# Performance work log

Hardware: AMD Instinct MI355X
Metric: run time of the kernel (lower is better)

Reference implementation:

```python
import jax, jax.numpy as jnp
import numpy as np

N_NODES = 100000
N_EDGES = 800000
EDGE_NAMES = ["ei_connected_to", "ei_ordered_next", "ei_represents", "ei_represented_by",
              "ei_neighboring_vertical", "ei_neighboring_horizontal", "ei_contains",
              "ei_order", "ei_perpendicular"]
AGGRS_L2 = ["sum", "sum", "mean", "mean", "sum", "sum", "mean"]


def _glorot(key, shape):
    fan_in, fan_out = shape[-2], shape[-1]
    s = (2.0 / (fan_in + fan_out)) ** 0.5
    return jax.random.normal(key, shape, dtype=jnp.float32) * s


def setup_inputs() -> dict:
    key = jax.random.key(0)
    ks = iter(jax.random.split(key, 32))
    inp = {"x": jax.random.normal(next(ks), (N_NODES, 6), dtype=jnp.float32)}
    for name in EDGE_NAMES:
        inp[name] = jax.random.randint(next(ks), (2, N_EDGES), 0, N_NODES, dtype=jnp.int32)
    inp.update(
        W0n=_glorot(next(ks), (2, 6, 16)), W0r=_glorot(next(ks), (2, 6, 16)),
        b0=jnp.zeros((2, 16), jnp.float32),
        W1n=_glorot(next(ks), (2, 16, 32)), W1r=_glorot(next(ks), (2, 16, 32)),
        b1=jnp.zeros((2, 32), jnp.float32),
        P1=_glorot(next(ks), (16, 32)), pb1=jnp.zeros((32,), jnp.float32),
        W2n=_glorot(next(ks), (7, 32, 64)), W2r=_glorot(next(ks), (7, 32, 64)),
        b2=jnp.zeros((7, 64), jnp.float32),
        P2=_glorot(next(ks), (32, 64)), pb2=jnp.zeros((64,), jnp.float32),
    )
    return inp


def _hetero_conv(x, edges, aggrs, Wn, Wr, b):
    # Per-relation GraphConv: out_d = aggr(x[src]->dst) @ Wn_r + x @ Wr_r + b_r,
    # summed across relations (HeteroConv aggr='sum'). Loop is over a small fixed
    # set of relation types (structurally distinct), not data dims.
    n = x.shape[0]
    out = jnp.zeros((n, Wn.shape[-1]), x.dtype)
    for i, (ei, aggr) in enumerate(zip(edges, aggrs)):
        src, dst = ei[0], ei[1]
        msg = jax.ops.segment_sum(x[src], dst, num_segments=n)  # scatter-add gather
        if aggr == "mean":
            cnt = jax.ops.segment_sum(jnp.ones_like(dst, dtype=x.dtype), dst, num_segments=n)
            msg = msg / jnp.maximum(cnt, 1.0)[:, None]
        out = out + msg @ Wn[i] + x @ Wr[i] + b[i]
    return out


def reference(x, W0n, W0r, b0, W1n, W1r, b1, P1, pb1, W2n, W2r, b2, P2, pb2,
              ei_connected_to, ei_ordered_next, ei_represents, ei_represented_by,
              ei_neighboring_vertical, ei_neighboring_horizontal, ei_contains,
              ei_order, ei_perpendicular):
    e01 = [ei_connected_to, ei_ordered_next]
    e2 = [ei_represents, ei_represented_by, ei_neighboring_vertical,
          ei_neighboring_horizontal, ei_contains, ei_order, ei_perpendicular]
    # local head: 6 -> 16 (two sum relations)
    h = _hetero_conv(x, e01, ["sum", "sum"], W0n, W0r, b0)
    # residual block 1: 16 -> 32 (same two sum relations, linear residual projection)
    h = jax.nn.relu(_hetero_conv(h, e01, ["sum", "sum"], W1n, W1r, b1) + h @ P1 + pb1)
    # residual block 2: 32 -> 64 (seven relations, sum/mean aggregation)
    h = jax.nn.relu(_hetero_conv(h, e2, AGGRS_L2, W2n, W2r, b2) + h @ P2 + pb2)
    # final elementwise relu from SemanticModule.forward
    return jax.nn.relu(h)
```

## Files before the change

### kernel.cpp

```cpp
#include <hip/hip_runtime.h>

#define NN 100000
#define NE 800000
#define NRG 256
#define SPAN 392
#define CAP 4096
#define NBIN (9 * NRG)
#define ACH 2048

typedef _Float16 f16;
typedef __attribute__((ext_vector_type(4))) _Float16 f16x4;
typedef __attribute__((ext_vector_type(8))) _Float16 f16x8;
typedef __attribute__((ext_vector_type(4))) float f32x4;
typedef __attribute__((ext_vector_type(2))) float f32x2;

#define NTL(p) __builtin_nontemporal_load(p)

struct EPtrs { const int* s[9]; const int* d[9]; };

__global__ __launch_bounds__(256) void prep_weights(
    const float* __restrict__ W0n, const float* __restrict__ W0r, const float* __restrict__ b0,
    const float* __restrict__ W1n, const float* __restrict__ W1r, const float* __restrict__ b1,
    const float* __restrict__ P1,  const float* __restrict__ pb1,
    const float* __restrict__ W2n, const float* __restrict__ W2r, const float* __restrict__ b2,
    const float* __restrict__ P2,  const float* __restrict__ pb2,
    float* __restrict__ wc0, float* __restrict__ bc0,
    float* __restrict__ wc1, float* __restrict__ bc1,
    f16*   __restrict__ b2frag, float* __restrict__ bc2,
    int*   __restrict__ cursor)
{
    int gtid = blockIdx.x * 256 + threadIdx.x;
    int gstr = gridDim.x * 256;

    for (int t = gtid; t < NBIN; t += gstr) cursor[t] = 0;

    for (int t = gtid; t < 18 * 16; t += gstr) {
        int row = t >> 4, col = t & 15;
        float v;
        if (row < 6)       v = W0n[row * 16 + col];
        else if (row < 12) v = W0n[96 + (row - 6) * 16 + col];
        else               v = W0r[(row - 12) * 16 + col] + W0r[96 + (row - 12) * 16 + col];
        wc0[t] = v;
    }
    for (int t = gtid; t < 16; t += gstr) bc0[t] = b0[t] + b0[16 + t];

    for (int t = gtid; t < 48 * 32; t += gstr) {
        int row = t >> 5, col = t & 31;
        float v;
        if (row < 16)      v = W1n[row * 32 + col];
        else if (row < 32) v = W1n[512 + (row - 16) * 32 + col];
        else { int rr = row - 32; v = W1r[rr * 32 + col] + W1r[512 + rr * 32 + col] + P1[rr * 32 + col]; }
        wc1[t] = v;
    }
    for (int t = gtid; t < 32; t += gstr) bc1[t] = b1[t] + b1[32 + t] + pb1[t];

    for (int t = gtid; t < 256 * 64; t += gstr) {
        int j = t & 7, lane = (t >> 3) & 63, ntk = t >> 9;
        int nt = ntk & 3, kt = ntk >> 2;
        int k = kt * 32 + (lane >> 4) * 8 + j;
        int n = nt * 16 + (lane & 15);
        float v;
        if (k < 224) v = W2n[k * 64 + n];
        else {
            int rr = k - 224;
            v = P2[rr * 64 + n];
            #pragma unroll
            for (int r = 0; r < 7; ++r) v += W2r[r * 2048 + rr * 64 + n];
        }
        b2frag[t] = (f16)v;
    }
    for (int t = gtid; t < 64; t += gstr) {
        float v = pb2[t];
        #pragma unroll
        for (int r = 0; r < 7; ++r) v += b2[r * 64 + t];
        bc2[t] = v;
    }
}

__global__ __launch_bounds__(256) void passA(EPtrs ep, int* __restrict__ cursor,
                                             unsigned* __restrict__ binbuf)
{
    int r = blockIdx.y;
    int e0 = blockIdx.x * ACH;
    int cnt = min(ACH, NE - e0);
    int tid = threadIdx.x;
    __shared__ int h[NRG];
    __shared__ int bs[NRG];
    __shared__ int gb[NRG];
    __shared__ int wsumA[4];
    __shared__ unsigned pk[ACH];
    __shared__ unsigned char pkb[ACH];

    h[tid] = 0;
    __syncthreads();

    const int* dp = ep.d[r];
    const int* sp = ep.s[r];
    unsigned wv[8];
    int rgk[8];
    int lrk[8];
    #pragma unroll
    for (int k = 0; k < 8; ++k) {
        int e = e0 + k * 256 + tid;
        rgk[k] = -1;
        if (e < NE) {
            int d = NTL(dp + e);
            int sv = NTL(sp + e);
            int g = d / SPAN;
            int l = d - g * SPAN;
            wv[k] = ((unsigned)l << 17) | (unsigned)sv;
            rgk[k] = g;
            lrk[k] = atomicAdd(&h[g], 1);
        }
    }
    __syncthreads();

    int vcnt = h[tid];
    int lane = tid & 63, wid = tid >> 6;
    int incl = vcnt;
    #pragma unroll
    for (int ofs = 1; ofs < 64; ofs <<= 1) {
        int u = __shfl_up(incl, ofs, 64);
        if (lane >= ofs) incl += u;
    }
    if (lane == 63) wsumA[wid] = incl;
    __syncthreads();
    if (tid == 0) {
        int a = wsumA[0], b = wsumA[1], c = wsumA[2];
        wsumA[0] = 0; wsumA[1] = a; wsumA[2] = a + b; wsumA[3] = a + b + c;
    }
    __syncthreads();
    int excl = incl - vcnt + wsumA[wid];
    bs[tid] = excl;
    gb[tid] = (vcnt > 0) ? atomicAdd(&cursor[r * NRG + tid], vcnt) : 0;
    __syncthreads();

    #pragma unroll
    for (int k = 0; k < 8; ++k) {
        if (rgk[k] >= 0) {
            int p = bs[rgk[k]] + lrk[k];
            pk[p] = wv[k];
            pkb[p] = (unsigned char)rgk[k];
        }
    }
    __syncthreads();

    for (int i = tid; i < cnt; i += 256) {
        int g = pkb[i];
        int pos = gb[g] + (i - bs[g]);
        if (pos < CAP)
            binbuf[((size_t)(r * NRG + g)) * CAP + pos] = pk[i];
    }
}

__global__ __launch_bounds__(256) void passB(const unsigned* __restrict__ binbuf,
                                             const int* __restrict__ cursor,
                                             int* __restrict__ deg, int* __restrict__ off,
                                             int* __restrict__ eidx)
{
    int bin = blockIdx.x;
    int r = bin >> 8, rg = bin & (NRG - 1);
    int lo = rg * SPAN;
    int n_here = min(SPAN, NN - lo);
    int tid = threadIdx.x;
    __shared__ int h[SPAN];
    __shared__ int wsum[4];
    __shared__ int stage[CAP];

    int sz = min(cursor[bin], CAP);
    const unsigned* bp = binbuf + (size_t)bin * CAP;

    for (int i = tid; i < SPAN; i += 256) h[i] = 0;
    __syncthreads();

    unsigned wv[16];
    int rk[16];
    #pragma unroll
    for (int k = 0; k < 16; ++k) {
        int e = tid + k * 256;
        if (e < sz) {
            unsigned w = NTL(bp + e);
            wv[k] = w;
            rk[k] = atomicAdd(&h[w >> 17], 1);
        }
    }
    __syncthreads();

    int i0 = tid * 2;
    int dstash[2];
    int s = 0;
    #pragma unroll
    for (int k = 0; k < 2; ++k) {
        int i = i0 + k;
        int v = (i < SPAN) ? h[i] : 0;
        dstash[k] = v;
        s += v;
    }
    int lane = tid & 63, wid = tid >> 6;
    int incl = s;
    #pragma unroll
    for (int ofs = 1; ofs < 64; ofs <<= 1) {
        int u = __shfl_up(incl, ofs, 64);
        if (lane >= ofs) incl += u;
    }
    if (lane == 63) wsum[wid] = incl;
    __syncthreads();
    if (tid == 0) {
        int a = wsum[0], b = wsum[1], c = wsum[2];
        wsum[0] = 0; wsum[1] = a; wsum[2] = a + b; wsum[3] = a + b + c;
    }
    __syncthreads();
    int run = incl - s + wsum[wid];
    int base = bin * CAP;
    #pragma unroll
    for (int k = 0; k < 2; ++k) {
        int i = i0 + k;
        if (i < SPAN) {
            int v = dstash[k];
            h[i] = run;
            if (i < n_here) {
                deg[r * NN + lo + i] = v;
                off[r * NN + lo + i] = base + run + v;
            }
            run += v;
        }
    }
    __syncthreads();

    #pragma unroll
    for (int k = 0; k < 16; ++k) {
        int e = tid + k * 256;
        if (e < sz) {
            unsigned w = wv[k];
            stage[h[w >> 17] + rk[k]] = (int)(w & 0x1FFFF);
        }
    }
    __syncthreads();
    for (int i = tid; i < sz; i += 256) eidx[base + i] = stage[i];
}

__global__ __launch_bounds__(256) void t0f(const float* __restrict__ x,
                                           const int* __restrict__ deg, const int* __restrict__ off,
                                           const int* __restrict__ eidx,
                                           const float* __restrict__ wc0, const float* __restrict__ bc0,
                                           f16* __restrict__ h0h)
{
    __shared__ float sw[288 + 16];
    for (int t = threadIdx.x; t < 304; t += 256) sw[t] = (t < 288) ? wc0[t] : bc0[t - 288];
    __syncthreads();
    int t = blockIdx.x * 256 + threadIdx.x;
    int node = t >> 2;
    if (node >= NN) return;
    int l = t & 3;
    int r = l >> 1, p = l & 1;

    float m[6] = {0, 0, 0, 0, 0, 0};
    {
        int e1 = off[r * NN + node];
        int e0 = e1 - deg[r * NN + node];
        int e = e0 + p;
        for (; e + 2 < e1; e += 4) {
            int sA = eidx[e], sB = eidx[e + 2];
            const float2* pA = reinterpret_cast<const float2*>(x + (size_t)sA * 6);
            const float2* pB = reinterpret_cast<const float2*>(x + (size_t)sB * 6);
            float2 a0 = pA[0], a1 = pA[1], a2 = pA[2];
            float2 b0 = pB[0], b1 = pB[1], b2 = pB[2];
            m[0] += a0.x + b0.x; m[1] += a0.y + b0.y;
            m[2] += a1.x + b1.x; m[3] += a1.y + b1.y;
            m[4] += a2.x + b2.x; m[5] += a2.y + b2.y;
        }
        if (e < e1) {
            int sA = eidx[e];
            const float2* pA = reinterpret_cast<const float2*>(x + (size_t)sA * 6);
            float2 a0 = pA[0], a1 = pA[1], a2 = pA[2];
            m[0] += a0.x; m[1] += a0.y; m[2] += a1.x; m[3] += a1.y; m[4] += a2.x; m[5] += a2.y;
        }
    }
    float mo[6];
    #pragma unroll
    for (int k = 0; k < 6; ++k) {
        m[k] += __shfl_xor(m[k], 1, 64);
        mo[k] = __shfl_xor(m[k], 2, 64);
    }
    int baseOwn = r * 96, baseOth = (1 - r) * 96;
    float xv[6];
    {
        const float2* xp = reinterpret_cast<const float2*>(x + (size_t)node * 6);
        float2 a = xp[0], b = xp[1], c = xp[2];
        xv[0] = a.x; xv[1] = a.y; xv[2] = b.x; xv[3] = b.y; xv[4] = c.x; xv[5] = c.y;
    }
    int dc = l * 4;
    float acc[4];
    #pragma unroll
    for (int j = 0; j < 4; ++j) acc[j] = sw[288 + dc + j];
    #pragma unroll
    for (int k = 0; k < 6; ++k) {
        #pragma unroll
        for (int j = 0; j < 4; ++j) {
            acc[j] = fmaf(m[k],  sw[baseOwn + k * 16 + dc + j], acc[j]);
            acc[j] = fmaf(mo[k], sw[baseOth + k * 16 + dc + j], acc[j]);
            acc[j] = fmaf(xv[k], sw[192 + k * 16 + dc + j], acc[j]);
        }
    }
    f16x4 o;
    #pragma unroll
    for (int j = 0; j < 4; ++j) o[j] = (f16)acc[j];
    *reinterpret_cast<f16x4*>(h0h + (size_t)node * 16 + dc) = o;
}

__global__ __launch_bounds__(256) void g1t(const int* __restrict__ deg, const int* __restrict__ off,
                                           const int* __restrict__ eidx, const f16* __restrict__ h0h,
                                           const float* __restrict__ wc1, const float* __restrict__ bc1,
                                           f16* __restrict__ h1h, unsigned* __restrict__ h1q)
{
    __shared__ float sw[1536 + 32];
    __shared__ float ms[32][33];
    for (int t = threadIdx.x; t < 1568; t += 256) sw[t] = (t < 1536) ? wc1[t] : bc1[t - 1536];

    int tid = threadIdx.x;
    int nloc = tid >> 3, l = tid & 7;
    int r = l >> 2, dq = l & 3;
    int node = blockIdx.x * 32 + nloc;

    if (node < NN) {
        int e1 = off[r * NN + node];
        int e0 = e1 - deg[r * NN + node];
        float a0 = 0.f, a1 = 0.f, a2 = 0.f, a3 = 0.f;
        int e = e0;
        for (; e + 4 <= e1; e += 4) {
            int sA = eidx[e], sB = eidx[e + 1], sC = eidx[e + 2], sD = eidx[e + 3];
            f16x4 vA = *reinterpret_cast<const f16x4*>(h0h + (size_t)sA * 16 + dq * 4);
            f16x4 vB = *reinterpret_cast<const f16x4*>(h0h + (size_t)sB * 16 + dq * 4);
            f16x4 vC = *reinterpret_cast<const f16x4*>(h0h + (size_t)sC * 16 + dq * 4);
            f16x4 vD = *reinterpret_cast<const f16x4*>(h0h + (size_t)sD * 16 + dq * 4);
            a0 += (float)vA[0] + (float)vB[0] + (float)vC[0] + (float)vD[0];
            a1 += (float)vA[1] + (float)vB[1] + (float)vC[1] + (float)vD[1];
            a2 += (float)vA[2] + (float)vB[2] + (float)vC[2] + (float)vD[2];
            a3 += (float)vA[3] + (float)vB[3] + (float)vC[3] + (float)vD[3];
        }
        for (; e < e1; ++e) {
            f16x4 v = *reinterpret_cast<const f16x4*>(h0h + (size_t)eidx[e] * 16 + dq * 4);
            a0 += (float)v[0]; a1 += (float)v[1]; a2 += (float)v[2]; a3 += (float)v[3];
        }
        ms[nloc][r * 16 + dq * 4 + 0] = a0;
        ms[nloc][r * 16 + dq * 4 + 1] = a1;
        ms[nloc][r * 16 + dq * 4 + 2] = a2;
        ms[nloc][r * 16 + dq * 4 + 3] = a3;
    }
    __syncthreads();
    if (node >= NN) return;

    int c0 = l * 4;
    float acc[4];
    #pragma unroll
    for (int j = 0; j < 4; ++j) acc[j] = sw[1536 + c0 + j];
    #pragma unroll
    for (int k = 0; k < 32; ++k) {
        float s = ms[nloc][k];
        #pragma unroll
        for (int j = 0; j < 4; ++j) acc[j] = fmaf(s, sw[k * 32 + c0 + j], acc[j]);
    }
    {
        const f16x8* hp = reinterpret_cast<const f16x8*>(h0h + (size_t)node * 16);
        f16x8 a = hp[0], b = hp[1];
        #pragma unroll
        for (int k = 0; k < 8; ++k) {
            float s0 = (float)a[k], s1 = (float)b[k];
            #pragma unroll
            for (int j = 0; j < 4; ++j)
                acc[j] = fmaf(s0, sw[(32 + k) * 32 + c0 + j], fmaf(s1, sw[(40 + k) * 32 + c0 + j], acc[j]));
        }
    }
    #pragma unroll
    for (int j = 0; j < 4; ++j) acc[j] = fmaxf(acc[j], 0.f);

    f16x4 o;
    #pragma unroll
    for (int j = 0; j < 4; ++j) o[j] = (f16)acc[j];
    *reinterpret_cast<f16x4*>(h1h + (size_t)node * 32 + c0) = o;

    int w0 = __builtin_amdgcn_cvt_pk_fp8_f32(acc[0], acc[1], 0, false);
    w0 = __builtin_amdgcn_cvt_pk_fp8_f32(acc[2], acc[3], w0, true);
    h1q[(size_t)node * 8 + l] = (unsigned)w0;
}

__global__ __launch_bounds__(256, 8) void g2t2(const int* __restrict__ deg, const int* __restrict__ off,
                                               const int* __restrict__ eidx, const unsigned* __restrict__ h1q,
                                               const f16* __restrict__ h1h, const f16* __restrict__ b2frag,
                                               const float* __restrict__ bc2, float* __restrict__ out)
{
    __shared__ f16 cat[16][264];

    int tid = threadIdx.x;
    int nloc = tid >> 4;
    int lane16 = tid & 15;
    int node = blockIdx.x * 16 + nloc;

    if (lane16 >= 14) {
        int part = lane16 - 14;
        const f16x8* hp = reinterpret_cast<const f16x8*>(h1h + (size_t)node * 32 + part * 16);
        f16x8 v0 = hp[0], v1 = hp[1];
        *reinterpret_cast<f16x8*>(&cat[nloc][224 + part * 16]) = v0;
        *reinterpret_cast<f16x8*>(&cat[nloc][224 + part * 16 + 8]) = v1;
    } else {
        int r = lane16 >> 1;
        int half = lane16 & 1;
        int d = deg[(r + 2) * NN + node];
        int e1 = off[(r + 2) * NN + node];
        int e0 = e1 - d;

        f32x2 acc[8];
        #pragma unroll
        for (int q = 0; q < 8; ++q) acc[q] = (f32x2){0.f, 0.f};

        const uint4* tbl = reinterpret_cast<const uint4*>(h1q);
        int e = e0;
        for (; e + 2 <= e1; e += 2) {
            int sA = eidx[e], sB = eidx[e + 1];
            uint4 qA = tbl[(size_t)sA * 2 + half];
            uint4 qB = tbl[(size_t)sB * 2 + half];
            acc[0] += __builtin_amdgcn_cvt_pk_f32_fp8(qA.x, false);
            acc[1] += __builtin_amdgcn_cvt_pk_f32_fp8(qA.x, true);
            acc[2] += __builtin_amdgcn_cvt_pk_f32_fp8(qA.y, false);
            acc[3] += __builtin_amdgcn_cvt_pk_f32_fp8(qA.y, true);
            acc[4] += __builtin_amdgcn_cvt_pk_f32_fp8(qA.z, false);
            acc[5] += __builtin_amdgcn_cvt_pk_f32_fp8(qA.z, true);
            acc[6] += __builtin_amdgcn_cvt_pk_f32_fp8(qA.w, false);
            acc[7] += __builtin_amdgcn_cvt_pk_f32_fp8(qA.w, true);
            acc[0] += __builtin_amdgcn_cvt_pk_f32_fp8(qB.x, false);
            acc[1] += __builtin_amdgcn_cvt_pk_f32_fp8(qB.x, true);
            acc[2] += __builtin_amdgcn_cvt_pk_f32_fp8(qB.y, false);
            acc[3] += __builtin_amdgcn_cvt_pk_f32_fp8(qB.y, true);
            acc[4] += __builtin_amdgcn_cvt_pk_f32_fp8(qB.z, false);
            acc[5] += __builtin_amdgcn_cvt_pk_f32_fp8(qB.z, true);
            acc[6] += __builtin_amdgcn_cvt_pk_f32_fp8(qB.w, false);
            acc[7] += __builtin_amdgcn_cvt_pk_f32_fp8(qB.w, true);
        }
        if (e < e1) {
            int sA = eidx[e];
            uint4 qA = tbl[(size_t)sA * 2 + half];
            acc[0] += __builtin_amdgcn_cvt_pk_f32_fp8(qA.x, false);
            acc[1] += __builtin_amdgcn_cvt_pk_f32_fp8(qA.x, true);
            acc[2] += __builtin_amdgcn_cvt_pk_f32_fp8(qA.y, false);
            acc[3] += __builtin_amdgcn_cvt_pk_f32_fp8(qA.y, true);
            acc[4] += __builtin_amdgcn_cvt_pk_f32_fp8(qA.z, false);
            acc[5] += __builtin_amdgcn_cvt_pk_f32_fp8(qA.z, true);
            acc[6] += __builtin_amdgcn_cvt_pk_f32_fp8(qA.w, false);
            acc[7] += __builtin_amdgcn_cvt_pk_f32_fp8(qA.w, true);
        }

        float sc = (r == 2 || r == 3 || r == 6) ? (1.0f / (float)max(d, 1)) : 1.0f;
        f16x8 o0, o1;
        #pragma unroll
        for (int q = 0; q < 4; ++q) {
            o0[q * 2 + 0] = (f16)(acc[q][0] * sc);
            o0[q * 2 + 1] = (f16)(acc[q][1] * sc);
            o1[q * 2 + 0] = (f16)(acc[4 + q][0] * sc);
            o1[q * 2 + 1] = (f16)(acc[4 + q][1] * sc);
        }
        *reinterpret_cast<f16x8*>(&cat[nloc][r * 32 + half * 16]) = o0;
        *reinterpret_cast<f16x8*>(&cat[nloc][r * 32 + half * 16 + 8]) = o1;
    }

    int lane = tid & 63, w = tid >> 6;
    int quad = lane >> 4, col0 = lane & 15;
    float bcv = bc2[w * 16 + col0];

    f16x8 bfr[8];
    #pragma unroll
    for (int kt = 0; kt < 8; ++kt)
        bfr[kt] = *reinterpret_cast<const f16x8*>(b2frag + ((size_t)(kt * 4 + w) * 64 + lane) * 8);

    __syncthreads();

    f32x4 acc = (f32x4){0.f, 0.f, 0.f, 0.f};
    #pragma unroll
    for (int kt = 0; kt < 8; ++kt) {
        f16x8 a = *reinterpret_cast<const f16x8*>(&cat[col0][kt * 32 + quad * 8]);
        acc = __builtin_amdgcn_mfma_f32_16x16x32_f16(a, bfr[kt], acc, 0, 0, 0);
    }

    int row0 = blockIdx.x * 16 + quad * 4;
    #pragma unroll
    for (int i = 0; i < 4; ++i)
        out[(size_t)(row0 + i) * 64 + w * 16 + col0] = fmaxf(acc[i] + bcv, 0.f);
}

extern "C" void kernel_launch(void* const* d_in, const int* in_sizes, int n_in,
                              void* d_out, int out_size, void* d_ws, size_t ws_size,
                              hipStream_t stream)
{
    const float* x = (const float*)d_in[0];
    EPtrs ep;
    for (int i = 0; i < 9; ++i) { const int* p = (const int*)d_in[1 + i]; ep.s[i] = p; ep.d[i] = p + NE; }
    const float* W0n = (const float*)d_in[10]; const float* W0r = (const float*)d_in[11];
    const float* b0  = (const float*)d_in[12];
    const float* W1n = (const float*)d_in[13]; const float* W1r = (const float*)d_in[14];
    const float* b1  = (const float*)d_in[15];
    const float* P1  = (const float*)d_in[16]; const float* pb1 = (const float*)d_in[17];
    const float* W2n = (const float*)d_in[18]; const float* W2r = (const float*)d_in[19];
    const float* b2  = (const float*)d_in[20];
    const float* P2  = (const float*)d_in[21]; const float* pb2 = (const float*)d_in[22];
    float* out = (float*)d_out;
    char* ws = (char*)d_ws;

    size_t off_b = 0;
    auto alloc = [&](size_t b) { size_t o = off_b; off_b += (b + 255) & ~(size_t)255; return o; };
    size_t o_wc0 = alloc(288 * 4);   size_t o_bc0 = alloc(16 * 4);
    size_t o_wc1 = alloc(1536 * 4);  size_t o_bc1 = alloc(32 * 4);
    size_t o_b2f = alloc(16384 * 2); size_t o_bc2 = alloc(64 * 4);
    size_t o_h0h = alloc((size_t)NN * 16 * 2);
    size_t o_h1q = alloc((size_t)NN * 32);
    size_t o_h1h = alloc((size_t)NN * 32 * 2);
    size_t o_bin = alloc((size_t)NBIN * CAP * 4);
    size_t o_deg = alloc((size_t)9 * NN * 4);
    size_t o_off = alloc((size_t)9 * NN * 4);
    size_t o_eid = alloc((size_t)NBIN * CAP * 4);
    size_t o_cur = alloc((size_t)NBIN * 4);
    (void)ws_size;

    float* wc0 = (float*)(ws + o_wc0); float* bc0 = (float*)(ws + o_bc0);
    float* wc1 = (float*)(ws + o_wc1); float* bc1 = (float*)(ws + o_bc1);
    f16*   b2f = (f16*)(ws + o_b2f);   float* bc2 = (float*)(ws + o_bc2);
    f16*   h0h = (f16*)(ws + o_h0h);
    unsigned* h1q = (unsigned*)(ws + o_h1q);
    f16*   h1h = (f16*)(ws + o_h1h);
    unsigned* binbuf = (unsigned*)(ws + o_bin);
    int*   deg = (int*)(ws + o_deg);
    int*   offp = (int*)(ws + o_off);
    int*   eid = (int*)(ws + o_eid);
    int*   cur = (int*)(ws + o_cur);

    dim3 B(256);
    prep_weights<<<32, B, 0, stream>>>(W0n, W0r, b0, W1n, W1r, b1, P1, pb1,
                                       W2n, W2r, b2, P2, pb2,
                                       wc0, bc0, wc1, bc1, b2f, bc2, cur);
    passA<<<dim3((NE + ACH - 1) / ACH, 9), B, 0, stream>>>(ep, cur, binbuf);
    passB<<<NBIN, B, 0, stream>>>(binbuf, cur, deg, offp, eid);

    t0f<<<(NN * 4 + 255) / 256, B, 0, stream>>>(x, deg, offp, eid, wc0, bc0, h0h);
    g1t<<<(NN + 31) / 32, B, 0, stream>>>(deg, offp, eid, h0h, wc1, bc1, h1h, h1q);
    g2t2<<<NN / 16, B, 0, stream>>>(deg, offp, eid, h1q, h1h, b2f, bc2, out);
}
```

Measured before the change: 279.5 us.

## Split g2t2 edge gather across two lanes per relation-half and halve launches

The layer-2 gather kernel now uses 512 threads per 16-node block, with two lanes sharing each (relation, half) edge list by taking alternate edges and combining partial sums through a lane shuffle. This doubles memory-level parallelism for the irregular fp8 gathers. Only four of the eight waves run the MFMA epilogue, and the grid is issued as two launches covering half the nodes each. The cost is idle waves during the matmul, shuffle overhead, and an extra kernel launch.

```diff
diff --git a/kernel.cpp b/kernel.cpp
--- a/kernel.cpp
+++ b/kernel.cpp
@@ -384,27 +384,27 @@
     h1q[(size_t)node * 8 + l] = (unsigned)w0;
 }
 
-__global__ __launch_bounds__(256, 8) void g2t2(const int* __restrict__ deg, const int* __restrict__ off,
+__global__ __launch_bounds__(512, 4) void g2t2(const int* __restrict__ deg, const int* __restrict__ off,
                                                const int* __restrict__ eidx, const unsigned* __restrict__ h1q,
                                                const f16* __restrict__ h1h, const f16* __restrict__ b2frag,
-                                               const float* __restrict__ bc2, float* __restrict__ out)
+                                               const float* __restrict__ bc2, float* __restrict__ out,
+                                               int nbase)
 {
     __shared__ f16 cat[16][264];
 
     int tid = threadIdx.x;
-    int nloc = tid >> 4;
-    int lane16 = tid & 15;
-    int node = blockIdx.x * 16 + nloc;
-
-    if (lane16 >= 14) {
-        int part = lane16 - 14;
-        const f16x8* hp = reinterpret_cast<const f16x8*>(h1h + (size_t)node * 32 + part * 16);
-        f16x8 v0 = hp[0], v1 = hp[1];
-        *reinterpret_cast<f16x8*>(&cat[nloc][224 + part * 16]) = v0;
-        *reinterpret_cast<f16x8*>(&cat[nloc][224 + part * 16 + 8]) = v1;
+    int nloc = tid >> 5;
+    int lane32 = tid & 31;
+    int node = nbase + blockIdx.x * 16 + nloc;
+
+    if (lane32 >= 28) {
+        int part = lane32 - 28;
+        f16x8 v = *reinterpret_cast<const f16x8*>(h1h + (size_t)node * 32 + part * 8);
+        *reinterpret_cast<f16x8*>(&cat[nloc][224 + part * 8]) = v;
     } else {
-        int r = lane16 >> 1;
-        int half = lane16 & 1;
+        int r = lane32 >> 2;
+        int half = (lane32 >> 1) & 1;
+        int par = lane32 & 1;
         int d = deg[(r + 2) * NN + node];
         int e1 = off[(r + 2) * NN + node];
         int e0 = e1 - d;
@@ -414,9 +414,9 @@
         for (int q = 0; q < 8; ++q) acc[q] = (f32x2){0.f, 0.f};
 
         const uint4* tbl = reinterpret_cast<const uint4*>(h1q);
-        int e = e0;
-        for (; e + 2 <= e1; e += 2) {
-            int sA = eidx[e], sB = eidx[e + 1];
+        int e = e0 + par;
+        for (; e + 2 < e1; e += 4) {
+            int sA = eidx[e], sB = eidx[e + 2];
             uint4 qA = tbl[(size_t)sA * 2 + half];
             uint4 qB = tbl[(size_t)sB * 2 + half];
             acc[0] += __builtin_amdgcn_cvt_pk_f32_fp8(qA.x, false);
@@ -449,29 +449,40 @@
             acc[7] += __builtin_amdgcn_cvt_pk_f32_fp8(qA.w, true);
         }
 
-        float sc = (r == 2 || r == 3 || r == 6) ? (1.0f / (float)max(d, 1)) : 1.0f;
-        f16x8 o0, o1;
-        #pragma unroll
-        for (int q = 0; q < 4; ++q) {
-            o0[q * 2 + 0] = (f16)(acc[q][0] * sc);
-            o0[q * 2 + 1] = (f16)(acc[q][1] * sc);
-            o1[q * 2 + 0] = (f16)(acc[4 + q][0] * sc);
-            o1[q * 2 + 1] = (f16)(acc[4 + q][1] * sc);
-        }
-        *reinterpret_cast<f16x8*>(&cat[nloc][r * 32 + half * 16]) = o0;
-        *reinterpret_cast<f16x8*>(&cat[nloc][r * 32 + half * 16 + 8]) = o1;
+        #pragma unroll
+        for (int q = 0; q < 8; ++q) {
+            acc[q][0] += __shfl_xor(acc[q][0], 1, 64);
+            acc[q][1] += __shfl_xor(acc[q][1], 1, 64);
+        }
+
+        if (par == 0) {
+            float sc = (r == 2 || r == 3 || r == 6) ? (1.0f / (float)max(d, 1)) : 1.0f;
+            f16x8 o0, o1;
+            #pragma unroll
+            for (int q = 0; q < 4; ++q) {
+                o0[q * 2 + 0] = (f16)(acc[q][0] * sc);
+                o0[q * 2 + 1] = (f16)(acc[q][1] * sc);
+                o1[q * 2 + 0] = (f16)(acc[4 + q][0] * sc);
+                o1[q * 2 + 1] = (f16)(acc[4 + q][1] * sc);
+            }
+            *reinterpret_cast<f16x8*>(&cat[nloc][r * 32 + half * 16]) = o0;
+            *reinterpret_cast<f16x8*>(&cat[nloc][r * 32 + half * 16 + 8]) = o1;
+        }
     }
 
     int lane = tid & 63, w = tid >> 6;
+    f16x8 bfr[8];
+    float bcv = 0.f;
     int quad = lane >> 4, col0 = lane & 15;
-    float bcv = bc2[w * 16 + col0];
-
-    f16x8 bfr[8];
-    #pragma unroll
-    for (int kt = 0; kt < 8; ++kt)
-        bfr[kt] = *reinterpret_cast<const f16x8*>(b2frag + ((size_t)(kt * 4 + w) * 64 + lane) * 8);
-
-    __syncthreads();
+    if (w < 4) {
+        bcv = bc2[w * 16 + col0];
+        #pragma unroll
+        for (int kt = 0; kt < 8; ++kt)
+            bfr[kt] = *reinterpret_cast<const f16x8*>(b2frag + ((size_t)(kt * 4 + w) * 64 + lane) * 8);
+    }
+
+    __syncthreads();
+    if (w >= 4) return;
 
     f32x4 acc = (f32x4){0.f, 0.f, 0.f, 0.f};
     #pragma unroll
@@ -480,7 +491,7 @@
         acc = __builtin_amdgcn_mfma_f32_16x16x32_f16(a, bfr[kt], acc, 0, 0, 0);
     }
 
-    int row0 = blockIdx.x * 16 + quad * 4;
+    int row0 = nbase + blockIdx.x * 16 + quad * 4;
     #pragma unroll
     for (int i = 0; i < 4; ++i)
         out[(size_t)(row0 + i) * 64 + w * 16 + col0] = fmaxf(acc[i] + bcv, 0.f);
@@ -532,6 +543,7 @@
     int*   cur = (int*)(ws + o_cur);
 
     dim3 B(256);
+    dim3 B2(512);
     prep_weights<<<32, B, 0, stream>>>(W0n, W0r, b0, W1n, W1r, b1, P1, pb1,
                                        W2n, W2r, b2, P2, pb2,
                                        wc0, bc0, wc1, bc1, b2f, bc2, cur);
@@ -540,5 +552,6 @@
 
     t0f<<<(NN * 4 + 255) / 256, B, 0, stream>>>(x, deg, offp, eid, wc0, bc0, h0h);
     g1t<<<(NN + 31) / 32, B, 0, stream>>>(deg, offp, eid, h0h, wc1, bc1, h1h, h1q);
-    g2t2<<<NN / 16, B, 0, stream>>>(deg, offp, eid, h1q, h1h, b2f, bc2, out);
-}
+    g2t2<<<NN / 32, B2, 0, stream>>>(deg, offp, eid, h1q, h1h, b2f, bc2, out, 0);
+    g2t2<<<NN / 32, B2, 0, stream>>>(deg, offp, eid, h1q, h1h, b2f, bc2, out, NN / 2);
+}
```

Measured after the change: 285.5 us. +2.1%, slower.
